# Optimization experiments

Hardware: AMD Instinct MI355X
Metric: run time of the kernel (lower is better)

Reference implementation:

```python
import jax, jax.numpy as jnp
import numpy as np

N = 50000      # nodes
E = 800000     # edges (avg degree 16)
C = 5000       # clusters (Kongming compression)
D = 128        # in_features
OUT = 40       # out_features (classes)
K = 2          # propagation hops


def setup_inputs() -> dict:
    key = jax.random.key(0)
    k1, k2, k3, k4, k5, k6 = jax.random.split(key, 6)
    x = jax.random.normal(k1, (N, D), dtype=jnp.float32)
    edge_index = jax.random.randint(k2, (2, E), 0, N, dtype=jnp.int32)
    cluster_index = jax.random.randint(k3, (N,), 0, C, dtype=jnp.int32)
    rep_idx = jax.random.randint(k4, (C,), 0, N, dtype=jnp.int32)
    W = jax.random.normal(k5, (OUT, D), dtype=jnp.float32) / np.sqrt(D)
    b = jax.random.normal(k6, (OUT,), dtype=jnp.float32) * 0.01
    return {"x": x, "edge_index": edge_index, "cluster_index": cluster_index,
            "rep_idx": rep_idx, "W": W, "b": b}


def _gcn_propagate(x, edge_index, k_hops):
    # PUPropagate: K hops of D^{-1/2}(A+I)D^{-1/2} x (gcn_norm with self-loops)
    n = x.shape[0]
    loops = jnp.arange(n, dtype=edge_index.dtype)
    src = jnp.concatenate([edge_index[0], loops])
    dst = jnp.concatenate([edge_index[1], loops])
    deg = jax.ops.segment_sum(jnp.ones_like(src, dtype=x.dtype), dst, num_segments=n)
    dinv = jnp.where(deg > 0, jax.lax.rsqrt(deg), 0.0)
    norm = (dinv[src] * dinv[dst])[:, None]            # [E+N, 1]
    h = x
    for _ in range(k_hops):                            # small fixed hop count
        h = jax.ops.segment_sum(h[src] * norm, dst, num_segments=n)
    return h


def reference(x, edge_index, cluster_index, rep_idx, W, b):
    h = _gcn_propagate(x, edge_index, K)               # [N, D]
    # Kongming_Cluster: gather one representative row per cluster
    hc = h[rep_idx]                                    # [C, D]
    yc = hc @ W.T + b                                  # [C, OUT] dense linear on compressed rows
    # Kongming_Reconstruct: scatter back to all nodes by cluster index
    y = yc[cluster_index]                              # [N, OUT]
    return jax.nn.log_softmax(y, axis=1)
```

## Files before the change

kernel.cpp:

```cpp
#include <hip/hip_runtime.h>
#include <math.h>

#define N_NODES 50000
#define N_EDGES 800000
#define N_CLUST 5000
#define DIM     128
#define NOUT    40
#define SLOTS   64

#define FILL_PART   8
#define NODES_PER_P (N_NODES / FILL_PART)
#define FILL_CHUNKS 100
#define EPC (N_EDGES / FILL_CHUNKS)

typedef __attribute__((ext_vector_type(8))) short short8;
typedef __attribute__((ext_vector_type(4))) float fvec4;
typedef __attribute__((ext_vector_type(4))) int ivec4;

__device__ __forceinline__ short bf16r(float v) {
    unsigned u = __float_as_uint(v);
    u = (u + 0x7FFFu + ((u >> 16) & 1u)) >> 16;
    return (short)u;
}
__device__ __forceinline__ unsigned pack_bf16x2(float a, float b) {
    unsigned ua = __float_as_uint(a);
    unsigned ub = __float_as_uint(b);
    ua = (ua + 0x7FFFu + ((ua >> 16) & 1u)) >> 16;
    ub = (ub + 0x7FFFu + ((ub >> 16) & 1u)) >> 16;
    return ua | (ub << 16);
}
__device__ __forceinline__ float2 unpack_bf16x2(unsigned v) {
    float2 r;
    r.x = __uint_as_float(v << 16);
    r.y = __uint_as_float(v & 0xFFFF0000u);
    return r;
}
__device__ __forceinline__ float4 unpack_bf16x4(uint2 v) {
    float4 r;
    r.x = __uint_as_float(v.x << 16);
    r.y = __uint_as_float(v.x & 0xFFFF0000u);
    r.z = __uint_as_float(v.y << 16);
    r.w = __uint_as_float(v.y & 0xFFFF0000u);
    return r;
}

__global__ __launch_bounds__(256) void fill_slots(const ivec4* __restrict__ src4,
                                                  const ivec4* __restrict__ dst4,
                                                  int* __restrict__ cnt,
                                                  unsigned short* __restrict__ slot) {
    int p = blockIdx.x & (FILL_PART - 1);
    int chunk = blockIdx.x >> 3;
    int lo = p * NODES_PER_P;
    int hi = lo + NODES_PER_P;
    int q0 = chunk * (EPC / 4);
    for (int i = threadIdx.x; i < EPC / 4; i += 256) {
        ivec4 d4 = __builtin_nontemporal_load(&dst4[q0 + i]);
        ivec4 s4 = __builtin_nontemporal_load(&src4[q0 + i]);
        if (d4.x >= lo && d4.x < hi) {
            int pos = atomicAdd(&cnt[d4.x], 1);
            if (pos < SLOTS) slot[d4.x * SLOTS + pos] = (unsigned short)s4.x;
        }
        if (d4.y >= lo && d4.y < hi) {
            int pos = atomicAdd(&cnt[d4.y], 1);
            if (pos < SLOTS) slot[d4.y * SLOTS + pos] = (unsigned short)s4.y;
        }
        if (d4.z >= lo && d4.z < hi) {
            int pos = atomicAdd(&cnt[d4.z], 1);
            if (pos < SLOTS) slot[d4.z * SLOTS + pos] = (unsigned short)s4.z;
        }
        if (d4.w >= lo && d4.w < hi) {
            int pos = atomicAdd(&cnt[d4.w], 1);
            if (pos < SLOTS) slot[d4.w * SLOTS + pos] = (unsigned short)s4.w;
        }
    }
}

__global__ __launch_bounds__(256) void zgemm(const float* __restrict__ x,
                                             const float* __restrict__ W,
                                             const int* __restrict__ cnt,
                                             unsigned short* __restrict__ zs) {
    int lane = threadIdx.x & 63;
    int wv = threadIdx.x >> 6;
    int q = lane >> 4, r16 = lane & 15;
    int tile = blockIdx.x * 4 + wv;
    if (tile >= N_NODES / 16) return;

    short8 bf[3][4];
    #pragma unroll
    for (int t = 0; t < 3; t++) {
        int o = t * 16 + r16;
        #pragma unroll
        for (int s = 0; s < 4; s++) {
            short8 f = {0, 0, 0, 0, 0, 0, 0, 0};
            if (o < NOUT) {
                const float* wp = W + o * DIM + s * 32 + q * 8;
                float4 w0 = *(const float4*)wp;
                float4 w1 = *(const float4*)(wp + 4);
                f[0] = bf16r(w0.x); f[1] = bf16r(w0.y);
                f[2] = bf16r(w0.z); f[3] = bf16r(w0.w);
                f[4] = bf16r(w1.x); f[5] = bf16r(w1.y);
                f[6] = bf16r(w1.z); f[7] = bf16r(w1.w);
            }
            bf[t][s] = f;
        }
    }

    int node = tile * 16 + r16;
    float dn = rsqrtf((float)cnt[node] + 1.0f);
    short8 af[4];
    #pragma unroll
    for (int s = 0; s < 4; s++) {
        const float* xp = x + (size_t)node * DIM + s * 32 + q * 8;
        float4 a0 = *(const float4*)xp;
        float4 a1 = *(const float4*)(xp + 4);
        short8 f;
        f[0] = bf16r(dn * a0.x); f[1] = bf16r(dn * a0.y);
        f[2] = bf16r(dn * a0.z); f[3] = bf16r(dn * a0.w);
        f[4] = bf16r(dn * a1.x); f[5] = bf16r(dn * a1.y);
        f[6] = bf16r(dn * a1.z); f[7] = bf16r(dn * a1.w);
        af[s] = f;
    }

    fvec4 acc0 = {0, 0, 0, 0}, acc1 = {0, 0, 0, 0}, acc2 = {0, 0, 0, 0};
    #pragma unroll
    for (int s = 0; s < 4; s++) {
        acc0 = __builtin_amdgcn_mfma_f32_16x16x32_bf16(af[s], bf[0][s], acc0, 0, 0, 0);
        acc1 = __builtin_amdgcn_mfma_f32_16x16x32_bf16(af[s], bf[1][s], acc1, 0, 0, 0);
        acc2 = __builtin_amdgcn_mfma_f32_16x16x32_bf16(af[s], bf[2][s], acc2, 0, 0, 0);
    }

    #pragma unroll
    for (int r = 0; r < 4; r++) {
        int nd = tile * 16 + q * 4 + r;
        unsigned short* zrow = zs + (size_t)nd * NOUT;
        zrow[r16]      = (unsigned short)bf16r(acc0[r]);
        zrow[16 + r16] = (unsigned short)bf16r(acc1[r]);
        if (r16 < 8) zrow[32 + r16] = (unsigned short)bf16r(acc2[r]);
    }
}

__global__ __launch_bounds__(256) void hop_all(const uint2* __restrict__ zs2,
                                               uint2* __restrict__ v12,
                                               const unsigned short* __restrict__ slot,
                                               const int* __restrict__ cnt) {
    int lane = threadIdx.x & 63;
    int g = lane / 10;
    int k = lane - g * 10;
    int wv = threadIdx.x >> 6;
    int n = blockIdx.x * 24 + wv * 6 + g;
    if (g >= 6 || n >= N_NODES) return;
    int c = cnt[n];
    int m = (c < SLOTS) ? c : SLOTS;
    float s = 1.0f / (float)(c + 1);
    float4 accA = unpack_bf16x4(zs2[n * 10 + k]);
    float4 accB; accB.x = accB.y = accB.z = accB.w = 0.0f;
    int base = n * SLOTS;
    int j = 0;
    for (; j + 3 < m; j += 4) {
        unsigned ss0 = *(const unsigned*)&slot[base + j];
        unsigned ss1 = *(const unsigned*)&slot[base + j + 2];
        float4 f0 = unpack_bf16x4(zs2[(int)(ss0 & 0xFFFFu) * 10 + k]);
        float4 f1 = unpack_bf16x4(zs2[(int)(ss0 >> 16) * 10 + k]);
        float4 f2 = unpack_bf16x4(zs2[(int)(ss1 & 0xFFFFu) * 10 + k]);
        float4 f3 = unpack_bf16x4(zs2[(int)(ss1 >> 16) * 10 + k]);
        accA.x += f0.x + f1.x;  accA.y += f0.y + f1.y;
        accA.z += f0.z + f1.z;  accA.w += f0.w + f1.w;
        accB.x += f2.x + f3.x;  accB.y += f2.y + f3.y;
        accB.z += f2.z + f3.z;  accB.w += f2.w + f3.w;
    }
    for (; j < m; j++) {
        float4 f0 = unpack_bf16x4(zs2[(int)slot[base + j] * 10 + k]);
        accB.x += f0.x; accB.y += f0.y; accB.z += f0.z; accB.w += f0.w;
    }
    uint2 p;
    p.x = pack_bf16x2(s * (accA.x + accB.x), s * (accA.y + accB.y));
    p.y = pack_bf16x2(s * (accA.z + accB.z), s * (accA.w + accB.w));
    v12[n * 10 + k] = p;
}

__global__ __launch_bounds__(256) void rep_lsm(const unsigned* __restrict__ v1,
                                               const unsigned short* __restrict__ slot,
                                               const int* __restrict__ cnt,
                                               const int* __restrict__ rep_idx,
                                               const float2* __restrict__ b2,
                                               float2* __restrict__ yc2) {
    int lane = threadIdx.x & 63;
    int wv = threadIdx.x >> 6;
    int c = blockIdx.x * 4 + wv;
    if (c >= N_CLUST) return;
    int n = rep_idx[c];
    int cn = cnt[n];
    int m = (cn < SLOTS) ? cn : SLOTS;
    float dn = rsqrtf((float)(cn + 1));
    int g = lane / 20;
    int k = lane - g * 20;
    float2 acc; acc.x = 0.0f; acc.y = 0.0f;
    if (g == 0) acc = unpack_bf16x2(v1[n * 20 + k]);
    if (g < 3) {
        int base = n * SLOTS;
        for (int j = g; j < m; j += 3) {
            float2 f = unpack_bf16x2(v1[(int)slot[base + j] * 20 + k]);
            acc.x += f.x; acc.y += f.y;
        }
    }
    float t1x = __shfl(acc.x, lane + 20), t1y = __shfl(acc.y, lane + 20);
    float t2x = __shfl(acc.x, lane + 40), t2y = __shfl(acc.y, lane + 40);
    bool act = (lane < 20);
    float2 h; h.x = 0.0f; h.y = 0.0f;
    if (act) {
        float2 bb = b2[k];
        h.x = dn * (acc.x + t1x + t2x) + bb.x;
        h.y = dn * (acc.y + t1y + t2y) + bb.y;
    }
    float mx = act ? fmaxf(h.x, h.y) : -INFINITY;
    #pragma unroll
    for (int off = 32; off; off >>= 1) mx = fmaxf(mx, __shfl_xor(mx, off));
    float e = act ? (expf(h.x - mx) + expf(h.y - mx)) : 0.0f;
    #pragma unroll
    for (int off = 32; off; off >>= 1) e += __shfl_xor(e, off);
    float lg = mx + logf(e);
    if (act) {
        float2 o; o.x = h.x - lg; o.y = h.y - lg;
        yc2[(size_t)c * 20 + k] = o;
    }
}

__global__ void gather_out(const float4* __restrict__ yc4, const int* __restrict__ cidx,
                           float4* __restrict__ out4) {
    int t = blockIdx.x * blockDim.x + threadIdx.x;
    if (t >= N_NODES * (NOUT / 4)) return;
    int n = t / (NOUT / 4);
    int q = t - n * (NOUT / 4);
    out4[t] = yc4[(size_t)cidx[n] * (NOUT / 4) + q];
}

extern "C" void kernel_launch(void* const* d_in, const int* in_sizes, int n_in,
                              void* d_out, int out_size, void* d_ws, size_t ws_size,
                              hipStream_t stream) {
    const float* x    = (const float*)d_in[0];
    const int*   esrc = (const int*)d_in[1];
    const int*   edst = ((const int*)d_in[1]) + N_EDGES;
    const int*   cidx = (const int*)d_in[2];
    const int*   ridx = (const int*)d_in[3];
    const float* W    = (const float*)d_in[4];
    const float* b    = (const float*)d_in[5];
    float* out = (float*)d_out;

    char* ws = (char*)d_ws;
    size_t off = 0;
    auto alloc = [&](size_t bytes) { char* p = ws + off; off += (bytes + 255) & ~size_t(255); return p; };
    int*            cnt  = (int*)alloc(N_NODES * 4);
    unsigned short* slot = (unsigned short*)alloc((size_t)N_NODES * SLOTS * 2);
    unsigned short* zs   = (unsigned short*)alloc((size_t)N_NODES * NOUT * 2);
    unsigned*       v1   = (unsigned*)alloc((size_t)N_NODES * (NOUT / 2) * 4);
    float*          yc   = (float*)alloc((size_t)N_CLUST * NOUT * 4);
    (void)ws_size; (void)in_sizes; (void)n_in; (void)out_size;

    hipMemsetAsync(cnt, 0, N_NODES * 4, stream);

    const int B = 256;
    fill_slots<<<FILL_PART * FILL_CHUNKS, 256, 0, stream>>>((const ivec4*)esrc,
                                                            (const ivec4*)edst,
                                                            cnt, slot);
    zgemm<<<(N_NODES / 16 + 3) / 4, 256, 0, stream>>>(x, W, cnt, zs);
    hop_all<<<(N_NODES + 23) / 24, 256, 0, stream>>>((const uint2*)zs, (uint2*)v1,
                                                     slot, cnt);
    rep_lsm<<<(N_CLUST + 3) / 4, 256, 0, stream>>>((const unsigned*)v1, slot, cnt, ridx,
                                                   (const float2*)b, (float2*)yc);
    int gt = N_NODES * (NOUT / 4);
    gather_out<<<(gt + B - 1) / B, B, 0, stream>>>((const float4*)yc, cidx, (float4*)out);
}
```

Before: 167.3 us.

## Fuse all stages into one persistent kernel with software grid barriers

Replaces the five separate kernel launches and the cnt memset with a single persistent kernel of 768 blocks. Stages are separated by an atomic-counter grid barrier, and each stage uses grid-stride loops. The aim is to remove launch gaps and the tail-drain cost between dependent stages. In exchange it needs all blocks co-resident to avoid deadlock, adds barrier spin overhead, and may lower per-stage parallelism compared with the larger original grids.

```diff
diff --git a/kernel.cpp b/kernel.cpp
--- a/kernel.cpp
+++ b/kernel.cpp
@@ -8,10 +8,18 @@
 #define NOUT    40
 #define SLOTS   64
 
+#define GRID_B   768
+#define NTHREADS (GRID_B * 256)
+#define NWAVES   (GRID_B * 4)
+
 #define FILL_PART   8
 #define NODES_PER_P (N_NODES / FILL_PART)
-#define FILL_CHUNKS 100
-#define EPC (N_EDGES / FILL_CHUNKS)
+#define FILL_CHUNKS 96
+#define EI4         (N_EDGES / 4)
+#define CI4         ((EI4 + FILL_CHUNKS - 1) / FILL_CHUNKS)
+
+#define ZTILES   (N_NODES / 16)
+#define HOPTASKS ((N_NODES + 5) / 6)
 
 typedef __attribute__((ext_vector_type(8))) short short8;
 typedef __attribute__((ext_vector_type(4))) float fvec4;
@@ -44,194 +52,229 @@
     return r;
 }
 
-__global__ __launch_bounds__(256) void fill_slots(const ivec4* __restrict__ src4,
-                                                  const ivec4* __restrict__ dst4,
-                                                  int* __restrict__ cnt,
-                                                  unsigned short* __restrict__ slot) {
-    int p = blockIdx.x & (FILL_PART - 1);
-    int chunk = blockIdx.x >> 3;
-    int lo = p * NODES_PER_P;
-    int hi = lo + NODES_PER_P;
-    int q0 = chunk * (EPC / 4);
-    for (int i = threadIdx.x; i < EPC / 4; i += 256) {
-        ivec4 d4 = __builtin_nontemporal_load(&dst4[q0 + i]);
-        ivec4 s4 = __builtin_nontemporal_load(&src4[q0 + i]);
-        if (d4.x >= lo && d4.x < hi) {
-            int pos = atomicAdd(&cnt[d4.x], 1);
-            if (pos < SLOTS) slot[d4.x * SLOTS + pos] = (unsigned short)s4.x;
-        }
-        if (d4.y >= lo && d4.y < hi) {
-            int pos = atomicAdd(&cnt[d4.y], 1);
-            if (pos < SLOTS) slot[d4.y * SLOTS + pos] = (unsigned short)s4.y;
-        }
-        if (d4.z >= lo && d4.z < hi) {
-            int pos = atomicAdd(&cnt[d4.z], 1);
-            if (pos < SLOTS) slot[d4.z * SLOTS + pos] = (unsigned short)s4.z;
-        }
-        if (d4.w >= lo && d4.w < hi) {
-            int pos = atomicAdd(&cnt[d4.w], 1);
-            if (pos < SLOTS) slot[d4.w * SLOTS + pos] = (unsigned short)s4.w;
-        }
-    }
-}
-
-__global__ __launch_bounds__(256) void zgemm(const float* __restrict__ x,
-                                             const float* __restrict__ W,
-                                             const int* __restrict__ cnt,
-                                             unsigned short* __restrict__ zs) {
+__device__ __forceinline__ void gbar(int* __restrict__ bar, int phase) {
+    __syncthreads();
+    if (threadIdx.x == 0) {
+        int* cnt = bar;
+        int* gen = bar + 32;
+        __threadfence();
+        if (atomicAdd(cnt, 1) == GRID_B - 1) {
+            atomicExch(cnt, 0);
+            __threadfence();
+            atomicExch(gen, phase);
+        } else {
+            while (atomicAdd(gen, 0) < phase) __builtin_amdgcn_s_sleep(8);
+        }
+        __threadfence();
+    }
+    __syncthreads();
+}
+
+__global__ __launch_bounds__(256, 4) void mega(const float* __restrict__ x,
+                                               const int* __restrict__ esrc,
+                                               const int* __restrict__ edst,
+                                               const int* __restrict__ cidx,
+                                               const int* __restrict__ ridx,
+                                               const float* __restrict__ W,
+                                               const float* __restrict__ b,
+                                               float* __restrict__ out,
+                                               int* __restrict__ bar,
+                                               int* __restrict__ cnt,
+                                               unsigned short* __restrict__ slot,
+                                               unsigned short* __restrict__ zs,
+                                               unsigned* __restrict__ v1,
+                                               float* __restrict__ yc) {
+    int tid  = blockIdx.x * 256 + threadIdx.x;
     int lane = threadIdx.x & 63;
-    int wv = threadIdx.x >> 6;
-    int q = lane >> 4, r16 = lane & 15;
-    int tile = blockIdx.x * 4 + wv;
-    if (tile >= N_NODES / 16) return;
-
-    short8 bf[3][4];
-    #pragma unroll
-    for (int t = 0; t < 3; t++) {
-        int o = t * 16 + r16;
-        #pragma unroll
-        for (int s = 0; s < 4; s++) {
-            short8 f = {0, 0, 0, 0, 0, 0, 0, 0};
-            if (o < NOUT) {
-                const float* wp = W + o * DIM + s * 32 + q * 8;
-                float4 w0 = *(const float4*)wp;
-                float4 w1 = *(const float4*)(wp + 4);
-                f[0] = bf16r(w0.x); f[1] = bf16r(w0.y);
-                f[2] = bf16r(w0.z); f[3] = bf16r(w0.w);
-                f[4] = bf16r(w1.x); f[5] = bf16r(w1.y);
-                f[6] = bf16r(w1.z); f[7] = bf16r(w1.w);
-            }
-            bf[t][s] = f;
-        }
-    }
-
-    int node = tile * 16 + r16;
-    float dn = rsqrtf((float)cnt[node] + 1.0f);
-    short8 af[4];
-    #pragma unroll
-    for (int s = 0; s < 4; s++) {
-        const float* xp = x + (size_t)node * DIM + s * 32 + q * 8;
-        float4 a0 = *(const float4*)xp;
-        float4 a1 = *(const float4*)(xp + 4);
-        short8 f;
-        f[0] = bf16r(dn * a0.x); f[1] = bf16r(dn * a0.y);
-        f[2] = bf16r(dn * a0.z); f[3] = bf16r(dn * a0.w);
-        f[4] = bf16r(dn * a1.x); f[5] = bf16r(dn * a1.y);
-        f[6] = bf16r(dn * a1.z); f[7] = bf16r(dn * a1.w);
-        af[s] = f;
-    }
-
-    fvec4 acc0 = {0, 0, 0, 0}, acc1 = {0, 0, 0, 0}, acc2 = {0, 0, 0, 0};
-    #pragma unroll
-    for (int s = 0; s < 4; s++) {
-        acc0 = __builtin_amdgcn_mfma_f32_16x16x32_bf16(af[s], bf[0][s], acc0, 0, 0, 0);
-        acc1 = __builtin_amdgcn_mfma_f32_16x16x32_bf16(af[s], bf[1][s], acc1, 0, 0, 0);
-        acc2 = __builtin_amdgcn_mfma_f32_16x16x32_bf16(af[s], bf[2][s], acc2, 0, 0, 0);
-    }
-
-    #pragma unroll
-    for (int r = 0; r < 4; r++) {
-        int nd = tile * 16 + q * 4 + r;
-        unsigned short* zrow = zs + (size_t)nd * NOUT;
-        zrow[r16]      = (unsigned short)bf16r(acc0[r]);
-        zrow[16 + r16] = (unsigned short)bf16r(acc1[r]);
-        if (r16 < 8) zrow[32 + r16] = (unsigned short)bf16r(acc2[r]);
-    }
-}
-
-__global__ __launch_bounds__(256) void hop_all(const uint2* __restrict__ zs2,
-                                               uint2* __restrict__ v12,
-                                               const unsigned short* __restrict__ slot,
-                                               const int* __restrict__ cnt) {
-    int lane = threadIdx.x & 63;
-    int g = lane / 10;
-    int k = lane - g * 10;
-    int wv = threadIdx.x >> 6;
-    int n = blockIdx.x * 24 + wv * 6 + g;
-    if (g >= 6 || n >= N_NODES) return;
-    int c = cnt[n];
-    int m = (c < SLOTS) ? c : SLOTS;
-    float s = 1.0f / (float)(c + 1);
-    float4 accA = unpack_bf16x4(zs2[n * 10 + k]);
-    float4 accB; accB.x = accB.y = accB.z = accB.w = 0.0f;
-    int base = n * SLOTS;
-    int j = 0;
-    for (; j + 3 < m; j += 4) {
-        unsigned ss0 = *(const unsigned*)&slot[base + j];
-        unsigned ss1 = *(const unsigned*)&slot[base + j + 2];
-        float4 f0 = unpack_bf16x4(zs2[(int)(ss0 & 0xFFFFu) * 10 + k]);
-        float4 f1 = unpack_bf16x4(zs2[(int)(ss0 >> 16) * 10 + k]);
-        float4 f2 = unpack_bf16x4(zs2[(int)(ss1 & 0xFFFFu) * 10 + k]);
-        float4 f3 = unpack_bf16x4(zs2[(int)(ss1 >> 16) * 10 + k]);
-        accA.x += f0.x + f1.x;  accA.y += f0.y + f1.y;
-        accA.z += f0.z + f1.z;  accA.w += f0.w + f1.w;
-        accB.x += f2.x + f3.x;  accB.y += f2.y + f3.y;
-        accB.z += f2.z + f3.z;  accB.w += f2.w + f3.w;
-    }
-    for (; j < m; j++) {
-        float4 f0 = unpack_bf16x4(zs2[(int)slot[base + j] * 10 + k]);
-        accB.x += f0.x; accB.y += f0.y; accB.z += f0.z; accB.w += f0.w;
-    }
-    uint2 p;
-    p.x = pack_bf16x2(s * (accA.x + accB.x), s * (accA.y + accB.y));
-    p.y = pack_bf16x2(s * (accA.z + accB.z), s * (accA.w + accB.w));
-    v12[n * 10 + k] = p;
-}
-
-__global__ __launch_bounds__(256) void rep_lsm(const unsigned* __restrict__ v1,
-                                               const unsigned short* __restrict__ slot,
-                                               const int* __restrict__ cnt,
-                                               const int* __restrict__ rep_idx,
-                                               const float2* __restrict__ b2,
-                                               float2* __restrict__ yc2) {
-    int lane = threadIdx.x & 63;
-    int wv = threadIdx.x >> 6;
-    int c = blockIdx.x * 4 + wv;
-    if (c >= N_CLUST) return;
-    int n = rep_idx[c];
-    int cn = cnt[n];
-    int m = (cn < SLOTS) ? cn : SLOTS;
-    float dn = rsqrtf((float)(cn + 1));
-    int g = lane / 20;
-    int k = lane - g * 20;
-    float2 acc; acc.x = 0.0f; acc.y = 0.0f;
-    if (g == 0) acc = unpack_bf16x2(v1[n * 20 + k]);
-    if (g < 3) {
-        int base = n * SLOTS;
-        for (int j = g; j < m; j += 3) {
-            float2 f = unpack_bf16x2(v1[(int)slot[base + j] * 20 + k]);
-            acc.x += f.x; acc.y += f.y;
-        }
-    }
-    float t1x = __shfl(acc.x, lane + 20), t1y = __shfl(acc.y, lane + 20);
-    float t2x = __shfl(acc.x, lane + 40), t2y = __shfl(acc.y, lane + 40);
-    bool act = (lane < 20);
-    float2 h; h.x = 0.0f; h.y = 0.0f;
-    if (act) {
-        float2 bb = b2[k];
-        h.x = dn * (acc.x + t1x + t2x) + bb.x;
-        h.y = dn * (acc.y + t1y + t2y) + bb.y;
-    }
-    float mx = act ? fmaxf(h.x, h.y) : -INFINITY;
-    #pragma unroll
-    for (int off = 32; off; off >>= 1) mx = fmaxf(mx, __shfl_xor(mx, off));
-    float e = act ? (expf(h.x - mx) + expf(h.y - mx)) : 0.0f;
-    #pragma unroll
-    for (int off = 32; off; off >>= 1) e += __shfl_xor(e, off);
-    float lg = mx + logf(e);
-    if (act) {
-        float2 o; o.x = h.x - lg; o.y = h.y - lg;
-        yc2[(size_t)c * 20 + k] = o;
-    }
-}
-
-__global__ void gather_out(const float4* __restrict__ yc4, const int* __restrict__ cidx,
-                           float4* __restrict__ out4) {
-    int t = blockIdx.x * blockDim.x + threadIdx.x;
-    if (t >= N_NODES * (NOUT / 4)) return;
-    int n = t / (NOUT / 4);
-    int q = t - n * (NOUT / 4);
-    out4[t] = yc4[(size_t)cidx[n] * (NOUT / 4) + q];
+    int wv   = threadIdx.x >> 6;
+    int gwave = blockIdx.x * 4 + wv;
+
+    for (int i = tid; i < N_NODES; i += NTHREADS) cnt[i] = 0;
+    gbar(bar, 1);
+
+    {
+        int p = blockIdx.x & (FILL_PART - 1);
+        int chunk = blockIdx.x >> 3;
+        int lo = p * NODES_PER_P;
+        int hi = lo + NODES_PER_P;
+        int c0 = chunk * CI4;
+        int c1 = (c0 + CI4 < EI4) ? c0 + CI4 : EI4;
+        const ivec4* src4 = (const ivec4*)esrc;
+        const ivec4* dst4 = (const ivec4*)edst;
+        for (int i = c0 + threadIdx.x; i < c1; i += 256) {
+            ivec4 d4 = __builtin_nontemporal_load(&dst4[i]);
+            ivec4 s4 = __builtin_nontemporal_load(&src4[i]);
+            if (d4.x >= lo && d4.x < hi) {
+                int pos = atomicAdd(&cnt[d4.x], 1);
+                if (pos < SLOTS) slot[d4.x * SLOTS + pos] = (unsigned short)s4.x;
+            }
+            if (d4.y >= lo && d4.y < hi) {
+                int pos = atomicAdd(&cnt[d4.y], 1);
+                if (pos < SLOTS) slot[d4.y * SLOTS + pos] = (unsigned short)s4.y;
+            }
+            if (d4.z >= lo && d4.z < hi) {
+                int pos = atomicAdd(&cnt[d4.z], 1);
+                if (pos < SLOTS) slot[d4.z * SLOTS + pos] = (unsigned short)s4.z;
+            }
+            if (d4.w >= lo && d4.w < hi) {
+                int pos = atomicAdd(&cnt[d4.w], 1);
+                if (pos < SLOTS) slot[d4.w * SLOTS + pos] = (unsigned short)s4.w;
+            }
+        }
+    }
+    gbar(bar, 2);
+
+    {
+        int q = lane >> 4, r16 = lane & 15;
+        for (int tile = gwave; tile < ZTILES; tile += NWAVES) {
+            short8 bfr[3][4];
+            #pragma unroll
+            for (int t = 0; t < 3; t++) {
+                int o = t * 16 + r16;
+                #pragma unroll
+                for (int s = 0; s < 4; s++) {
+                    short8 f = {0, 0, 0, 0, 0, 0, 0, 0};
+                    if (o < NOUT) {
+                        const float* wp = W + o * DIM + s * 32 + q * 8;
+                        float4 w0 = *(const float4*)wp;
+                        float4 w1 = *(const float4*)(wp + 4);
+                        f[0] = bf16r(w0.x); f[1] = bf16r(w0.y);
+                        f[2] = bf16r(w0.z); f[3] = bf16r(w0.w);
+                        f[4] = bf16r(w1.x); f[5] = bf16r(w1.y);
+                        f[6] = bf16r(w1.z); f[7] = bf16r(w1.w);
+                    }
+                    bfr[t][s] = f;
+                }
+            }
+
+            int node = tile * 16 + r16;
+            float dn = rsqrtf((float)cnt[node] + 1.0f);
+            short8 af[4];
+            #pragma unroll
+            for (int s = 0; s < 4; s++) {
+                const float* xp = x + (size_t)node * DIM + s * 32 + q * 8;
+                float4 a0 = *(const float4*)xp;
+                float4 a1 = *(const float4*)(xp + 4);
+                short8 f;
+                f[0] = bf16r(dn * a0.x); f[1] = bf16r(dn * a0.y);
+                f[2] = bf16r(dn * a0.z); f[3] = bf16r(dn * a0.w);
+                f[4] = bf16r(dn * a1.x); f[5] = bf16r(dn * a1.y);
+                f[6] = bf16r(dn * a1.z); f[7] = bf16r(dn * a1.w);
+                af[s] = f;
+            }
+
+            fvec4 acc0 = {0, 0, 0, 0}, acc1 = {0, 0, 0, 0}, acc2 = {0, 0, 0, 0};
+            #pragma unroll
+            for (int s = 0; s < 4; s++) {
+                acc0 = __builtin_amdgcn_mfma_f32_16x16x32_bf16(af[s], bfr[0][s], acc0, 0, 0, 0);
+                acc1 = __builtin_amdgcn_mfma_f32_16x16x32_bf16(af[s], bfr[1][s], acc1, 0, 0, 0);
+                acc2 = __builtin_amdgcn_mfma_f32_16x16x32_bf16(af[s], bfr[2][s], acc2, 0, 0, 0);
+            }
+
+            #pragma unroll
+            for (int r = 0; r < 4; r++) {
+                int nd = tile * 16 + q * 4 + r;
+                unsigned short* zrow = zs + (size_t)nd * NOUT;
+                zrow[r16]      = (unsigned short)bf16r(acc0[r]);
+                zrow[16 + r16] = (unsigned short)bf16r(acc1[r]);
+                if (r16 < 8) zrow[32 + r16] = (unsigned short)bf16r(acc2[r]);
+            }
+        }
+    }
+    gbar(bar, 3);
+
+    {
+        const uint2* zs2 = (const uint2*)zs;
+        uint2* v12 = (uint2*)v1;
+        int g = lane / 10;
+        int k = lane - g * 10;
+        for (int t = gwave; t < HOPTASKS; t += NWAVES) {
+            int n = t * 6 + g;
+            if (g < 6 && n < N_NODES) {
+                int c = cnt[n];
+                int m = (c < SLOTS) ? c : SLOTS;
+                float s = 1.0f / (float)(c + 1);
+                float4 accA = unpack_bf16x4(zs2[n * 10 + k]);
+                float4 accB; accB.x = accB.y = accB.z = accB.w = 0.0f;
+                int base = n * SLOTS;
+                int j = 0;
+                for (; j + 3 < m; j += 4) {
+                    unsigned ss0 = *(const unsigned*)&slot[base + j];
+                    unsigned ss1 = *(const unsigned*)&slot[base + j + 2];
+                    float4 f0 = unpack_bf16x4(zs2[(int)(ss0 & 0xFFFFu) * 10 + k]);
+                    float4 f1 = unpack_bf16x4(zs2[(int)(ss0 >> 16) * 10 + k]);
+                    float4 f2 = unpack_bf16x4(zs2[(int)(ss1 & 0xFFFFu) * 10 + k]);
+                    float4 f3 = unpack_bf16x4(zs2[(int)(ss1 >> 16) * 10 + k]);
+                    accA.x += f0.x + f1.x;  accA.y += f0.y + f1.y;
+                    accA.z += f0.z + f1.z;  accA.w += f0.w + f1.w;
+                    accB.x += f2.x + f3.x;  accB.y += f2.y + f3.y;
+                    accB.z += f2.z + f3.z;  accB.w += f2.w + f3.w;
+                }
+                for (; j < m; j++) {
+                    float4 f0 = unpack_bf16x4(zs2[(int)slot[base + j] * 10 + k]);
+                    accB.x += f0.x; accB.y += f0.y; accB.z += f0.z; accB.w += f0.w;
+                }
+                uint2 pk;
+                pk.x = pack_bf16x2(s * (accA.x + accB.x), s * (accA.y + accB.y));
+                pk.y = pack_bf16x2(s * (accA.z + accB.z), s * (accA.w + accB.w));
+                v12[n * 10 + k] = pk;
+            }
+        }
+    }
+    gbar(bar, 4);
+
+    {
+        const float2* b2 = (const float2*)b;
+        float2* yc2 = (float2*)yc;
+        int g = lane / 20;
+        int k = lane - g * 20;
+        for (int c = gwave; c < N_CLUST; c += NWAVES) {
+            int n = ridx[c];
+            int cn = cnt[n];
+            int m = (cn < SLOTS) ? cn : SLOTS;
+            float dn = rsqrtf((float)(cn + 1));
+            float2 acc; acc.x = 0.0f; acc.y = 0.0f;
+            if (g == 0) acc = unpack_bf16x2(v1[n * 20 + k]);
+            if (g < 3) {
+                int base = n * SLOTS;
+                for (int j = g; j < m; j += 3) {
+                    float2 f = unpack_bf16x2(v1[(int)slot[base + j] * 20 + k]);
+                    acc.x += f.x; acc.y += f.y;
+                }
+            }
+            float t1x = __shfl(acc.x, lane + 20), t1y = __shfl(acc.y, lane + 20);
+            float t2x = __shfl(acc.x, lane + 40), t2y = __shfl(acc.y, lane + 40);
+            bool act = (lane < 20);
+            float2 h; h.x = 0.0f; h.y = 0.0f;
+            if (act) {
+                float2 bb = b2[k];
+                h.x = dn * (acc.x + t1x + t2x) + bb.x;
+                h.y = dn * (acc.y + t1y + t2y) + bb.y;
+            }
+            float mx = act ? fmaxf(h.x, h.y) : -INFINITY;
+            #pragma unroll
+            for (int off = 32; off; off >>= 1) mx = fmaxf(mx, __shfl_xor(mx, off));
+            float e = act ? (expf(h.x - mx) + expf(h.y - mx)) : 0.0f;
+            #pragma unroll
+            for (int off = 32; off; off >>= 1) e += __shfl_xor(e, off);
+            float lg = mx + logf(e);
+            if (act) {
+                float2 o; o.x = h.x - lg; o.y = h.y - lg;
+                yc2[(size_t)c * 20 + k] = o;
+            }
+        }
+    }
+    gbar(bar, 5);
+
+    {
+        const float4* yc4 = (const float4*)yc;
+        float4* out4 = (float4*)out;
+        for (int t = tid; t < N_NODES * (NOUT / 4); t += NTHREADS) {
+            int n = t / (NOUT / 4);
+            int q = t - n * (NOUT / 4);
+            out4[t] = yc4[(size_t)cidx[n] * (NOUT / 4) + q];
+        }
+    }
 }
 
 extern "C" void kernel_launch(void* const* d_in, const int* in_sizes, int n_in,
@@ -249,6 +292,7 @@
     char* ws = (char*)d_ws;
     size_t off = 0;
     auto alloc = [&](size_t bytes) { char* p = ws + off; off += (bytes + 255) & ~size_t(255); return p; };
+    int*            bar  = (int*)alloc(256);
     int*            cnt  = (int*)alloc(N_NODES * 4);
     unsigned short* slot = (unsigned short*)alloc((size_t)N_NODES * SLOTS * 2);
     unsigned short* zs   = (unsigned short*)alloc((size_t)N_NODES * NOUT * 2);
@@ -256,17 +300,8 @@
     float*          yc   = (float*)alloc((size_t)N_CLUST * NOUT * 4);
     (void)ws_size; (void)in_sizes; (void)n_in; (void)out_size;
 
-    hipMemsetAsync(cnt, 0, N_NODES * 4, stream);
-
-    const int B = 256;
-    fill_slots<<<FILL_PART * FILL_CHUNKS, 256, 0, stream>>>((const ivec4*)esrc,
-                                                            (const ivec4*)edst,
-                                                            cnt, slot);
-    zgemm<<<(N_NODES / 16 + 3) / 4, 256, 0, stream>>>(x, W, cnt, zs);
-    hop_all<<<(N_NODES + 23) / 24, 256, 0, stream>>>((const uint2*)zs, (uint2*)v1,
-                                                     slot, cnt);
-    rep_lsm<<<(N_CLUST + 3) / 4, 256, 0, stream>>>((const unsigned*)v1, slot, cnt, ridx,
-                                                   (const float2*)b, (float2*)yc);
-    int gt = N_NODES * (NOUT / 4);
-    gather_out<<<(gt + B - 1) / B, B, 0, stream>>>((const float4*)yc, cidx, (float4*)out);
-}
+    hipMemsetAsync(bar, 0, 256, stream);
+
+    mega<<<GRID_B, 256, 0, stream>>>(x, esrc, edst, cidx, ridx, W, b, out,
+                                     bar, cnt, slot, zs, v1, yc);
+}
```

Result: slower. 317.0 us (+89.5%).
